# Kernel tuning notes

Hardware: AMD Instinct MI355X
Metric: run time of the kernel (lower is better)

The kernel has to match this reference:

```python
import math
import jax, jax.numpy as jnp
from jax import lax
import numpy as np

PATCHES = [(8, 8), (4, 4), (2, 2), (1, 1)]  # (width, height) per scale
BN_EPS = 1e-5


def setup_inputs() -> dict:
    key = jax.random.key(0)
    ks = jax.random.split(key, 9)
    b, d, h, w = 4, 256, 64, 64
    s = 1.0 / math.sqrt(d)
    return {
        "x": jax.random.normal(ks[0], (b, d, h, w), jnp.float32),
        "wq": jax.random.normal(ks[1], (d, d), jnp.float32) * s,
        "bq": jax.random.normal(ks[2], (d,), jnp.float32) * 0.02,
        "wk": jax.random.normal(ks[3], (d, d), jnp.float32) * s,
        "bk": jax.random.normal(ks[4], (d,), jnp.float32) * 0.02,
        "wv": jax.random.normal(ks[5], (d, d), jnp.float32) * s,
        "bv": jax.random.normal(ks[6], (d,), jnp.float32) * 0.02,
        "w_out": jax.random.normal(ks[7], (d, d, 3, 3), jnp.float32) * (s / 3.0),
        "b_out": jax.random.normal(ks[8], (d,), jnp.float32) * 0.02,
        "gamma": jnp.ones((d,), jnp.float32),
        "beta": jnp.zeros((d,), jnp.float32),
    }


def _to_tokens(t, b, dk, out_h, ph, out_w, pw):
    # [b, dk, h, w] -> [b, out_h*out_w, dk*ph*pw]
    t = t.reshape(b, dk, out_h, ph, out_w, pw)
    t = t.transpose(0, 2, 4, 1, 3, 5)
    return t.reshape(b, out_h * out_w, dk * ph * pw)


def reference(x, wq, bq, wk, bk, wv, bv, w_out, b_out, gamma, beta):
    b, c, h, w = x.shape
    # 1x1 conv projections == channel matmuls
    q = jnp.einsum('bchw,oc->bohw', x, wq) + bq[None, :, None, None]
    k = jnp.einsum('bchw,oc->bohw', x, wk) + bk[None, :, None, None]
    v = jnp.einsum('bchw,oc->bohw', x, wv) + bv[None, :, None, None]

    dk = c // len(PATCHES)
    outs = []
    for i, (pw, ph) in enumerate(PATCHES):
        sl = slice(i * dk, (i + 1) * dk)
        out_h, out_w = h // ph, w // pw
        Q = _to_tokens(q[:, sl], b, dk, out_h, ph, out_w, pw)
        K = _to_tokens(k[:, sl], b, dk, out_h, ph, out_w, pw)
        V = _to_tokens(v[:, sl], b, dk, out_h, ph, out_w, pw)
        scores = jnp.einsum('bnd,bmd->bnm', Q, K) / math.sqrt(Q.shape[-1])
        p = jax.nn.softmax(scores, axis=-1)
        y = jnp.einsum('bnm,bmd->bnd', p, V)
        # tokens -> [b, dk, h, w]
        y = y.reshape(b, out_h, out_w, dk, ph, pw)
        y = y.transpose(0, 3, 1, 4, 2, 5).reshape(b, dk, h, w)
        outs.append(y)
    out = jnp.concatenate(outs, axis=1)

    # 3x3 conv, padding=1
    z = lax.conv_general_dilated(out, w_out, (1, 1), 'SAME',
                                 dimension_numbers=('NCHW', 'OIHW', 'NCHW'))
    z = z + b_out[None, :, None, None]
    # BatchNorm2d (training-mode batch stats)
    mean = jnp.mean(z, axis=(0, 2, 3), keepdims=True)
    var = jnp.var(z, axis=(0, 2, 3), keepdims=True)
    zn = (z - mean) * lax.rsqrt(var + BN_EPS)
    zn = zn * gamma[None, :, None, None] + beta[None, :, None, None]
    # LeakyReLU(0.2)
    return jnp.where(zn > 0, zn, 0.2 * zn)
```

## Files before the change

kernel.cpp:

```cpp
#include <hip/hip_runtime.h>
#include <cmath>


#define OFF_XB  0LL
#define OFF_QB  2097152LL
#define OFF_SS  8388608LL
#define OFF_PP  12582912LL
#define OFF_YT  14680064LL
#define OFF_WQK 18874368LL
#define OFF_BIA 18972672LL
#define OFF_WCV 18973440LL
#define OFF_STT 19268352LL

#define FC 0.18033688f
#define CSHIFT 6.0f

typedef __attribute__((ext_vector_type(8))) short short8;
typedef __attribute__((ext_vector_type(4))) float f32x4;

__device__ inline unsigned short f2bf(float f) {
  unsigned u = __float_as_uint(f);
  u += 0x7fff + ((u >> 16) & 1);
  return (unsigned short)(u >> 16);
}

__device__ inline unsigned cvt_pk_bf16(float a, float b) {
  unsigned r;
  asm("v_cvt_pk_bf16_f32 %0, %1, %2" : "=v"(r) : "v"(a), "v"(b));
  return r;
}

__global__ __launch_bounds__(256) void xpose_k(
    const float* __restrict__ x, unsigned short* __restrict__ xb)
{
  __shared__ unsigned short rowb[256][66];
  const int b = blockIdx.x >> 6, y = blockIdx.x & 63;
  const int t = threadIdx.x;
  for (int i = t; i < 16384; i += 256) {
    int c = i >> 6, xx = i & 63;
    rowb[c][xx] = f2bf(x[((long long)(b*256 + c) << 12) + (y << 6) + xx]);
  }
  __syncthreads();
  unsigned int* outw = (unsigned int*)(xb + ((long long)blockIdx.x << 14));
  for (int i = t; i < 8192; i += 256) {
    int xx = i >> 7, c2 = (i & 127) * 2;
    outw[xx*128 + (c2 >> 1)] = (unsigned)rowb[c2][xx]
                             | ((unsigned)rowb[c2+1][xx] << 16);
  }
}

__global__ __launch_bounds__(256) void wcvt_k(
    const float* __restrict__ wq, const float* __restrict__ wk,
    const float* __restrict__ wv, const float* __restrict__ bq,
    const float* __restrict__ bk, const float* __restrict__ bv,
    unsigned short* __restrict__ Wqkv, float* __restrict__ biasQKV)
{
  const int row = blockIdx.x, t = threadIdx.x;
  const int which = row >> 8, oc = row & 255;
  const float* src = which == 0 ? wq : which == 1 ? wk : wv;
  Wqkv[row*256 + t] = f2bf(src[oc*256 + t]);
  if (row < 3) {
    const float* bs = row == 0 ? bq : row == 1 ? bk : bv;
    biasQKV[row*256 + t] = bs[t];
  }
}

template<int EPI, int ONEW>
__global__ __launch_bounds__(ONEW ? 64 : 256) void gemm_nt_k(
    const unsigned short* __restrict__ A, const unsigned short* __restrict__ B,
    void* __restrict__ Cv, const float* __restrict__ bias,
    int M, int N, int K, int lda, int ldb, int ldc,
    long long sA, long long sB, long long sC, float alpha)
{
  const int t = threadIdx.x, l = t & 63;
  const int lr = l & 15, lg = l >> 4;
  const int w = ONEW ? 0 : (t >> 6);
  const int wm = w >> 1, wn = w & 1;
  const int bz = blockIdx.z;
  const int m0 = blockIdx.y*(ONEW ? 64 : 128) + wm*64;
  const int n0 = blockIdx.x*(ONEW ? 64 : 128) + wn*64;
  if (m0 >= M || n0 >= N) return;
  const unsigned short* Ab = A + (long long)bz*sA + (long long)(m0 + lr)*lda + lg*8;
  const unsigned short* Bb = B + (long long)bz*sB + (long long)(n0 + lr)*ldb + lg*8;

  f32x4 acc[4][4] = {};
#pragma unroll 2
  for (int kk = 0; kk < K; kk += 32) {
    short8 af[4], bf[4];
#pragma unroll
    for (int i = 0; i < 4; i++)
      af[i] = *(const short8*)(Ab + (long long)i*16*lda + kk);
#pragma unroll
    for (int i = 0; i < 4; i++)
      bf[i] = *(const short8*)(Bb + (long long)i*16*ldb + kk);
#pragma unroll
    for (int mf = 0; mf < 4; mf++)
#pragma unroll
      for (int nf = 0; nf < 4; nf++)
        acc[mf][nf] = __builtin_amdgcn_mfma_f32_16x16x32_bf16(
            af[mf], bf[nf], acc[mf][nf], 0, 0, 0);
  }

  if (EPI == 0) {
    float* C = (float*)Cv + (long long)bz*sC;
#pragma unroll
    for (int mf = 0; mf < 4; mf++)
#pragma unroll
      for (int r = 0; r < 4; r++) {
        const int row = m0 + mf*16 + lg*4 + r;
#pragma unroll
        for (int nf = 0; nf < 4; nf++)
          C[(long long)row*ldc + n0 + nf*16 + lr] = acc[mf][nf][r] * alpha;
      }
  } else {
    unsigned short* Qbase = (unsigned short*)Cv;
#pragma unroll
    for (int mf = 0; mf < 4; mf++)
#pragma unroll
      for (int r = 0; r < 4; r++) {
        const int gi = m0 + mf*16 + lg*4 + r;
        const int which = gi >> 8, ch = gi & 255;
        const int scale = ch >> 6, c = ch & 63;
        const int sh = 3 - scale, msk = (1 << sh) - 1;
        const bool tr = (which == 2);
        const float bb = bias[gi];
        unsigned short* dst = Qbase + (long long)which*4194304
                            + (long long)scale*1048576 + (long long)bz*262144;
#pragma unroll
        for (int nf = 0; nf < 4; nf++) {
          const int gj = n0 + nf*16 + lr;
          const int y = gj >> 6, xx = gj & 63;
          const int n = (y >> sh)*(64 >> sh) + (xx >> sh);
          const int d = (c << (2*sh)) + ((y & msk) << sh) + (xx & msk);
          const long long idx = tr
              ? (long long)d*(4096 >> (2*sh)) + n
              : (long long)n*(64 << (2*sh)) + d;
          dst[idx] = f2bf(acc[mf][nf][r] + bb);
        }
      }
  }
}

__global__ __launch_bounds__(256) void s0_scores_k(
    const unsigned short* __restrict__ Q, const unsigned short* __restrict__ K,
    float* __restrict__ Sp)
{
  __shared__ float red[3][64][64];
  const int t = threadIdx.x, l = t & 63, w = t >> 6;
  const int lr = l & 15, lg = l >> 4;
  const int b = blockIdx.x >> 3, ks = blockIdx.x & 7;
  const unsigned short* Qb = Q + (long long)b*262144;
  const unsigned short* Kb = K + (long long)b*262144;
  f32x4 acc[4][4] = {};
  const int k0 = ks*512 + w*128;
#pragma unroll
  for (int kk = k0; kk < k0 + 128; kk += 32) {
    short8 af[4], bf[4];
#pragma unroll
    for (int i = 0; i < 4; i++)
      af[i] = *(const short8*)(Qb + (long long)(i*16 + lr)*4096 + kk + lg*8);
#pragma unroll
    for (int i = 0; i < 4; i++)
      bf[i] = *(const short8*)(Kb + (long long)(i*16 + lr)*4096 + kk + lg*8);
#pragma unroll
    for (int mf = 0; mf < 4; mf++)
#pragma unroll
      for (int nf = 0; nf < 4; nf++)
        acc[mf][nf] = __builtin_amdgcn_mfma_f32_16x16x32_bf16(
            af[mf], bf[nf], acc[mf][nf], 0, 0, 0);
  }
  if (w > 0) {
#pragma unroll
    for (int mf = 0; mf < 4; mf++)
#pragma unroll
      for (int r = 0; r < 4; r++)
#pragma unroll
        for (int nf = 0; nf < 4; nf++)
          red[w-1][mf*16 + lg*4 + r][nf*16 + lr] = acc[mf][nf][r];
  }
  __syncthreads();
  if (w == 0) {
#pragma unroll
    for (int mf = 0; mf < 4; mf++)
#pragma unroll
      for (int r = 0; r < 4; r++) {
        const int row = mf*16 + lg*4 + r;
#pragma unroll
        for (int nf = 0; nf < 4; nf++) {
          const int col = nf*16 + lr;
          Sp[(((long long)(ks*4 + b)*64 + row) << 6) + col]
              = acc[mf][nf][r] + red[0][row][col] + red[1][row][col]
              + red[2][row][col];
        }
      }
  }
}

__global__ __launch_bounds__(256) void s0_softmax_k(
    const float* __restrict__ Sp, unsigned short* __restrict__ P)
{
  const int t = threadIdx.x, l = t & 63, w = t >> 6;
  const int row = blockIdx.x*4 + w;
  const int b = row >> 6, r = row & 63;
  float v = 0.f;
#pragma unroll
  for (int ks = 0; ks < 8; ks++)
    v += Sp[(((long long)(ks*4 + b)*64 + r) << 6) + l];
  v *= 0.015625f;
  float mx = v;
#pragma unroll
  for (int off = 1; off < 64; off <<= 1) mx = fmaxf(mx, __shfl_xor(mx, off, 64));
  float e = __expf(v - mx), sum = e;
#pragma unroll
  for (int off = 1; off < 64; off <<= 1) sum += __shfl_xor(sum, off, 64);
  P[(row << 6) + l] = f2bf(e / sum);
}

template<int CNT>
__global__ __launch_bounds__(256) void softmax_bf_k(
    const float* __restrict__ S, unsigned short* __restrict__ P)
{
  const int t = threadIdx.x, l = t & 63, w = t >> 6;
  const long long row = (long long)blockIdx.x*4 + w;
  const float* p = S + row*(CNT*64);
  unsigned short* o = P + row*(CNT*64);
  float v[CNT];
  float mx = -1e30f;
#pragma unroll
  for (int i = 0; i < CNT; i++) { v[i] = p[i*64 + l]; mx = fmaxf(mx, v[i]); }
#pragma unroll
  for (int off = 1; off < 64; off <<= 1) mx = fmaxf(mx, __shfl_xor(mx, off, 64));
  float sum = 0.f;
#pragma unroll
  for (int i = 0; i < CNT; i++) { v[i] = __expf(v[i] - mx); sum += v[i]; }
#pragma unroll
  for (int off = 1; off < 64; off <<= 1) sum += __shfl_xor(sum, off, 64);
  const float inv = 1.f / sum;
#pragma unroll
  for (int i = 0; i < CNT; i++) o[i*64 + l] = f2bf(v[i] * inv);
}

__global__ __launch_bounds__(256) void flash3_mfma_k(
    const unsigned short* __restrict__ Q3, const unsigned short* __restrict__ K3,
    const unsigned short* __restrict__ Vt3, float* __restrict__ part,
    float* __restrict__ ml)
{
  constexpr int LD = 72;
  __shared__ unsigned short Ks[64*LD];
  __shared__ unsigned short Vs[64*LD];
  __shared__ unsigned short Ps[64*LD];
  const int t = threadIdx.x, l = t & 63, w = t >> 6;
  const int lr = l & 15, lg = l >> 4;
  const int b = blockIdx.y, q0 = blockIdx.x * 64, sp = blockIdx.z;
  const long long base = (long long)b * 262144;
  const unsigned short* Qg = Q3 + base;
  const unsigned short* Kg = K3 + base;
  const unsigned short* Vg = Vt3 + base;

  short8 bq[2];
  bq[0] = *(const short8*)(Qg + (long long)(q0 + w*16 + lr)*64 + lg*8);
  bq[1] = *(const short8*)(Qg + (long long)(q0 + w*16 + lr)*64 + 32 + lg*8);

  f32x4 acc[4] = {};
  float li = 0.f;

  const int r_ = t >> 3, c8_ = (t & 7) * 8;
  for (int kt = sp*16; kt < sp*16 + 16; kt++) {
    const int k0 = kt * 64;
    __syncthreads();
#pragma unroll
    for (int it = 0; it < 2; it++) {
      const int rr = r_ + it*32;
      *(uint4*)(Ks + rr*LD + c8_) =
          *(const uint4*)(Kg + (long long)(k0 + rr)*64 + c8_);
      *(uint4*)(Vs + rr*LD + c8_) =
          *(const uint4*)(Vg + (long long)rr*4096 + k0 + c8_);
    }
    __syncthreads();
    f32x4 s[4];
#pragma unroll
    for (int cf = 0; cf < 4; cf++) {
      short8 ak0 = *(const short8*)(Ks + (cf*16 + lr)*LD + lg*8);
      short8 ak1 = *(const short8*)(Ks + (cf*16 + lr)*LD + 32 + lg*8);
      f32x4 zz = {};
      zz = __builtin_amdgcn_mfma_f32_16x16x32_bf16(ak0, bq[0], zz, 0,0,0);
      s[cf] = __builtin_amdgcn_mfma_f32_16x16x32_bf16(ak1, bq[1], zz, 0,0,0);
    }
    float p[16];
    float psum = 0.f;
#pragma unroll
    for (int cf = 0; cf < 4; cf++)
#pragma unroll
      for (int r = 0; r < 4; r++) {
        float e = exp2f(fmaf(s[cf][r], FC, -CSHIFT));
        p[cf*4 + r] = e; psum += e;
      }
    li += psum;
    {
      unsigned short* pr = Ps + (w*16 + lr)*LD;
#pragma unroll
      for (int cf = 0; cf < 4; cf++) {
        *(unsigned*)(pr + cf*16 + lg*4)     = cvt_pk_bf16(p[cf*4+0], p[cf*4+1]);
        *(unsigned*)(pr + cf*16 + lg*4 + 2) = cvt_pk_bf16(p[cf*4+2], p[cf*4+3]);
      }
    }
    short8 bp0 = *(const short8*)(Ps + (w*16 + lr)*LD + lg*8);
    short8 bp1 = *(const short8*)(Ps + (w*16 + lr)*LD + 32 + lg*8);
#pragma unroll
    for (int df = 0; df < 4; df++) {
      short8 av0 = *(const short8*)(Vs + (df*16 + lr)*LD + lg*8);
      short8 av1 = *(const short8*)(Vs + (df*16 + lr)*LD + 32 + lg*8);
      acc[df] = __builtin_amdgcn_mfma_f32_16x16x32_bf16(av0, bp0, acc[df], 0,0,0);
      acc[df] = __builtin_amdgcn_mfma_f32_16x16x32_bf16(av1, bp1, acc[df], 0,0,0);
    }
  }
  li += __shfl_xor(li, 16);
  li += __shfl_xor(li, 32);
  const long long prow = (long long)(sp*4 + b)*4096 + q0 + w*16 + lr;
#pragma unroll
  for (int df = 0; df < 4; df++)
    *(float4*)(part + prow*64 + df*16 + lg*4) =
        make_float4(acc[df][0], acc[df][1], acc[df][2], acc[df][3]);
  if (lg == 0) ml[prow] = li;
}

__global__ __launch_bounds__(256) void fcomb_k(
    const float* __restrict__ part, const float* __restrict__ ml,
    unsigned short* __restrict__ inb)
{
  const int t = threadIdx.x;
  const long long row = (long long)blockIdx.x*64 + (t >> 2);
  const int dd = (t & 3) * 16;
  float L = 0.f;
#pragma unroll
  for (int s = 0; s < 4; s++) L += ml[(long long)s*16384 + row];
  const float inv = 1.f / L;
#pragma unroll
  for (int j = 0; j < 4; j++) {
    float ax = 0.f, ay = 0.f, az = 0.f, aw = 0.f;
#pragma unroll
    for (int s = 0; s < 4; s++) {
      float4 v = *(const float4*)(part + ((long long)s*16384 + row)*64 + dd + j*4);
      ax += v.x; ay += v.y; az += v.z; aw += v.w;
    }
    ushort4 ov;
    ov.x = f2bf(ax*inv); ov.y = f2bf(ay*inv);
    ov.z = f2bf(az*inv); ov.w = f2bf(aw*inv);
    *(ushort4*)(inb + row*256 + 192 + dd + j*4) = ov;
  }
}

__global__ __launch_bounds__(256) void unpack_nhwc_k(
    const float* __restrict__ Yt, unsigned short* __restrict__ inb)
{
  __shared__ unsigned short rowb[192][66];
  const int b = blockIdx.x >> 6, y = blockIdx.x & 63;
  const int t = threadIdx.x;
  for (int i = t; i < 12288; i += 256) {
    int ch = i >> 6, x = i & 63;
    int scale = ch >> 6, c = ch & 63;
    int sh = 3 - scale, msk = (1 << sh) - 1;
    int n = (y >> sh) * (64 >> sh) + (x >> sh);
    int d = (c << (2*sh)) + ((y & msk) << sh) + (x & msk);
    rowb[ch][x] = f2bf(Yt[(long long)scale*1048576 + ((long long)b << 18)
                          + (long long)n * (64 << (2*sh)) + d]);
  }
  __syncthreads();
  unsigned int* outw = (unsigned int*)(inb + ((long long)blockIdx.x << 14));
  for (int i = t; i < 6144; i += 256) {
    int xx = i / 96, cw = i % 96;
    outw[xx*128 + cw] = (unsigned)rowb[cw*2][xx]
                      | ((unsigned)rowb[cw*2+1][xx] << 16);
  }
}

__global__ __launch_bounds__(256) void wconv_k(
    const float* __restrict__ w, unsigned short* __restrict__ Wb)
{
  int i = blockIdx.x*256 + threadIdx.x;
  int tap = i >> 16, oc = (i >> 8) & 255, ic = i & 255;
  Wb[i] = f2bf(w[((long long)(oc*256 + ic))*9 + tap]);
}

__global__ __launch_bounds__(512) void conv_mfma_k(
    const unsigned short* __restrict__ inb, const unsigned short* __restrict__ Wb,
    const float* __restrict__ bias, float* __restrict__ z)
{
  __shared__ unsigned short lds[6*66*40];
  const int t = threadIdx.x;
  const int l = t & 63, wid = t >> 6;
  const int waveM = wid >> 2, waveN = wid & 3;
  const int tile = blockIdx.x;
  const int b = tile >> 4, y0 = (tile & 15) * 4;
  const int oc0 = blockIdx.y * 64 + waveM * 32;
  const long long inbase = (long long)b * 1048576;

  f32x4 acc[2][4] = {};

  const int kgrp = (l >> 4) * 8;
  for (int ic0 = 0; ic0 < 256; ic0 += 32) {
    __syncthreads();
    for (int q = t; q < 1584; q += 512) {
      int ic8 = q & 3, c = (q >> 2) % 66, r = q / 264;
      int gy = y0 - 1 + r, gx = c - 1;
      uint4 v = make_uint4(0u, 0u, 0u, 0u);
      if ((unsigned)gy < 64u && (unsigned)gx < 64u)
        v = *(const uint4*)(inb + inbase + ((long long)(gy*64 + gx))*256
                            + ic0 + ic8*8);
      *(uint4*)(lds + (q >> 2)*40 + ic8*8) = v;
    }
    __syncthreads();
    const unsigned short* wbase =
        Wb + (long long)(oc0 + (l & 15)) * 256 + ic0 + kgrp;
#pragma unroll
    for (int ky = 0; ky < 3; ky++) {
#pragma unroll
      for (int kx = 0; kx < 3; kx++) {
        const int tap = ky*3 + kx;
        short8 a0 = *(const short8*)(wbase + (long long)tap*65536);
        short8 a1 = *(const short8*)(wbase + (long long)tap*65536 + 16*256);
#pragma unroll
        for (int nf = 0; nf < 4; nf++) {
          int pix = waveN*64 + nf*16 + (l & 15);
          int rp = pix >> 6, x = pix & 63;
          short8 bf = *(const short8*)(lds + ((rp + ky)*66 + x + kx)*40 + kgrp);
          acc[0][nf] = __builtin_amdgcn_mfma_f32_16x16x32_bf16(a0, bf, acc[0][nf], 0, 0, 0);
          acc[1][nf] = __builtin_amdgcn_mfma_f32_16x16x32_bf16(a1, bf, acc[1][nf], 0, 0, 0);
        }
      }
    }
  }
  const long long zb = ((long long)b * 256) << 12;
#pragma unroll
  for (int mf = 0; mf < 2; mf++) {
#pragma unroll
    for (int r = 0; r < 4; r++) {
      const int oc = oc0 + mf*16 + (l >> 4)*4 + r;
      const float bb = bias[oc];
      const long long rowbase = zb + ((long long)oc << 12) + y0*64;
#pragma unroll
      for (int nf = 0; nf < 4; nf++) {
        int pix = waveN*64 + nf*16 + (l & 15);
        z[rowbase + pix] = acc[mf][nf][r] + bb;
      }
    }
  }
}

__global__ __launch_bounds__(256) void bn_stats_k(
    const float* __restrict__ z, float* __restrict__ stats)
{
  const int ch = blockIdx.x, t = threadIdx.x;
  float s = 0.f, q = 0.f;
  for (int b = 0; b < 4; b++) {
    const float* p = z + ((long long)(b*256 + ch) << 12);
    for (int i = t; i < 4096; i += 256) { float v = p[i]; s += v; q += v*v; }
  }
  __shared__ float rs[256], rq[256];
  rs[t] = s; rq[t] = q; __syncthreads();
  for (int st = 128; st > 0; st >>= 1) {
    if (t < st) { rs[t] += rs[t+st]; rq[t] += rq[t+st]; }
    __syncthreads();
  }
  if (t == 0) {
    float mean = rs[0] * (1.f/16384.f);
    float var  = rq[0] * (1.f/16384.f) - mean*mean;
    stats[ch]       = mean;
    stats[256 + ch] = rsqrtf(var + 1e-5f);
  }
}

__global__ __launch_bounds__(256) void bn_apply_k(
    const float* __restrict__ z, const float* __restrict__ stats,
    const float* __restrict__ gamma, const float* __restrict__ beta,
    float* __restrict__ out)
{
  long long i4 = ((long long)blockIdx.x*256 + threadIdx.x) * 4;
  int ch = (int)((i4 >> 12) & 255);
  float mean = stats[ch], rsg = stats[256 + ch];
  float g = gamma[ch], bt = beta[ch];
  float4 v = *(const float4*)(z + i4);
  float r[4] = {v.x, v.y, v.z, v.w};
#pragma unroll
  for (int j = 0; j < 4; j++) {
    float u = (r[j] - mean) * rsg * g + bt;
    r[j] = u > 0.f ? u : 0.2f * u;
  }
  *(float4*)(out + i4) = make_float4(r[0], r[1], r[2], r[3]);
}

extern "C" void kernel_launch(void* const* d_in, const int* in_sizes, int n_in,
                              void* d_out, int out_size, void* d_ws, size_t ws_size,
                              hipStream_t stream)
{
  const float* x     = (const float*)d_in[0];
  const float* wq    = (const float*)d_in[1];
  const float* bq    = (const float*)d_in[2];
  const float* wk    = (const float*)d_in[3];
  const float* bk    = (const float*)d_in[4];
  const float* wv    = (const float*)d_in[5];
  const float* bv    = (const float*)d_in[6];
  const float* w_out = (const float*)d_in[7];
  const float* b_out = (const float*)d_in[8];
  const float* gamma = (const float*)d_in[9];
  const float* beta  = (const float*)d_in[10];
  float* out = (float*)d_out;

  float* ws = (float*)d_ws;
  unsigned short* xb  = (unsigned short*)(ws + OFF_XB);
  unsigned short* Qu  = (unsigned short*)(ws + OFF_QB);
  unsigned short* Ku  = Qu + 4194304;
  unsigned short* Vu  = Qu + 8388608;
  float* SSf = ws + OFF_SS;
  unsigned short* PPu = (unsigned short*)(ws + OFF_PP);
  float* Yt  = ws + OFF_YT;
  unsigned short* Wqk = (unsigned short*)(ws + OFF_WQK);
  float* biasQ = ws + OFF_BIA;
  unsigned short* Wcv = (unsigned short*)(ws + OFF_WCV);
  float* St = ws + OFF_STT;
  unsigned short* inb = (unsigned short*)(ws + OFF_XB);
  float* z = Yt;

  dim3 blk(256);
  dim3 blk1(64);

  xpose_k<<<dim3(256), blk, 0, stream>>>(x, xb);
  wcvt_k<<<dim3(768), blk, 0, stream>>>(wq, wk, wv, bq, bk, bv, Wqk, biasQ);
  wconv_k<<<dim3(2304), blk, 0, stream>>>(w_out, Wcv);

  gemm_nt_k<1,0><<<dim3(32,6,4), blk, 0, stream>>>(
      Wqk, xb, (void*)Qu, biasQ, 768, 4096, 256, 256, 256, 0,
      0, 1048576, 0, 1.0f);

  s0_scores_k<<<dim3(32), blk, 0, stream>>>(Qu, Ku, SSf);
  s0_softmax_k<<<dim3(64), blk, 0, stream>>>(SSf, PPu);
  gemm_nt_k<0,1><<<dim3(64,1,4), blk1, 0, stream>>>(
      PPu, Vu, (void*)Yt, nullptr, 64, 4096, 64, 64, 64, 4096,
      4096, 262144, 262144, 1.0f);

  gemm_nt_k<0,1><<<dim3(4,4,4), blk1, 0, stream>>>(
      Qu+1048576, Ku+1048576, (void*)SSf, nullptr, 256, 256, 1024,
      1024, 1024, 256, 262144, 262144, 65536, 0.03125f);
  softmax_bf_k<4><<<dim3(256), blk, 0, stream>>>(SSf, PPu);
  gemm_nt_k<0,1><<<dim3(16,4,4), blk1, 0, stream>>>(
      PPu, Vu+1048576, (void*)(Yt+1048576), nullptr, 256, 1024, 256,
      256, 256, 1024, 65536, 262144, 262144, 1.0f);

  gemm_nt_k<0,0><<<dim3(8,8,4), blk, 0, stream>>>(
      Qu+2097152, Ku+2097152, (void*)SSf, nullptr, 1024, 1024, 256,
      256, 256, 1024, 262144, 262144, 1048576, 0.0625f);
  softmax_bf_k<16><<<dim3(1024), blk, 0, stream>>>(SSf, PPu);
  gemm_nt_k<0,1><<<dim3(4,16,4), blk1, 0, stream>>>(
      PPu, Vu+2097152, (void*)(Yt+2097152), nullptr, 1024, 256, 1024,
      1024, 1024, 256, 1048576, 262144, 262144, 1.0f);

  flash3_mfma_k<<<dim3(64,4,4), blk, 0, stream>>>(
      Qu+3145728, Ku+3145728, Vu+3145728, SSf, ws + OFF_PP);
  fcomb_k<<<dim3(256), blk, 0, stream>>>(SSf, ws + OFF_PP, inb);

  unpack_nhwc_k<<<dim3(256), blk, 0, stream>>>(Yt, inb);

  conv_mfma_k<<<dim3(64,4), dim3(512), 0, stream>>>(inb, Wcv, b_out, z);

  bn_stats_k<<<dim3(256), blk, 0, stream>>>(z, St);
  bn_apply_k<<<dim3(4096), blk, 0, stream>>>(z, St, gamma, beta, out);
}
```

Measured before the change: 266.7 us.

## Merge per-scale attention launches into staged multi-role kernels and double-buffer LDS loads

The separate prep kernels are merged into one launch. The per-scale score, softmax and PV kernels are grouped into three stage kernels that dispatch work by block index, so the scales run concurrently and launch count drops. The finest-scale flash attention now processes all keys in one block with register-staged double-buffered K/V, which removes the split-K partial buffers and the combine kernel. The 3x3 conv also gains double-buffered LDS and weights preloaded into registers. Risks include higher register pressure, lower parallelism for the flash blocks (256 blocks doing 64 iterations each), and load imbalance between the roles inside each stage kernel.

```diff
diff --git a/kernel.cpp b/kernel.cpp
--- a/kernel.cpp
+++ b/kernel.cpp
@@ -11,6 +11,10 @@
 #define OFF_BIA 18972672LL
 #define OFF_WCV 18973440LL
 #define OFF_STT 19268352LL
+#define OFF_SP0 19268864LL
+#define OFF_S1  19399936LL
+#define OFF_P0  19662080LL
+#define OFF_P1  19670272LL
 
 #define FC 0.18033688f
 #define CSHIFT 6.0f
@@ -30,55 +34,57 @@
   return r;
 }
 
-__global__ __launch_bounds__(256) void xpose_k(
-    const float* __restrict__ x, unsigned short* __restrict__ xb)
-{
-  __shared__ unsigned short rowb[256][66];
-  const int b = blockIdx.x >> 6, y = blockIdx.x & 63;
-  const int t = threadIdx.x;
-  for (int i = t; i < 16384; i += 256) {
-    int c = i >> 6, xx = i & 63;
-    rowb[c][xx] = f2bf(x[((long long)(b*256 + c) << 12) + (y << 6) + xx]);
-  }
-  __syncthreads();
-  unsigned int* outw = (unsigned int*)(xb + ((long long)blockIdx.x << 14));
-  for (int i = t; i < 8192; i += 256) {
-    int xx = i >> 7, c2 = (i & 127) * 2;
-    outw[xx*128 + (c2 >> 1)] = (unsigned)rowb[c2][xx]
-                             | ((unsigned)rowb[c2+1][xx] << 16);
-  }
-}
-
-__global__ __launch_bounds__(256) void wcvt_k(
+__global__ __launch_bounds__(256) void prep_k(
+    const float* __restrict__ x, unsigned short* __restrict__ xb,
     const float* __restrict__ wq, const float* __restrict__ wk,
     const float* __restrict__ wv, const float* __restrict__ bq,
     const float* __restrict__ bk, const float* __restrict__ bv,
-    unsigned short* __restrict__ Wqkv, float* __restrict__ biasQKV)
-{
-  const int row = blockIdx.x, t = threadIdx.x;
-  const int which = row >> 8, oc = row & 255;
-  const float* src = which == 0 ? wq : which == 1 ? wk : wv;
-  Wqkv[row*256 + t] = f2bf(src[oc*256 + t]);
-  if (row < 3) {
-    const float* bs = row == 0 ? bq : row == 1 ? bk : bv;
-    biasQKV[row*256 + t] = bs[t];
-  }
-}
-
-template<int EPI, int ONEW>
-__global__ __launch_bounds__(ONEW ? 64 : 256) void gemm_nt_k(
+    unsigned short* __restrict__ Wqkv, float* __restrict__ biasQKV,
+    const float* __restrict__ wcv, unsigned short* __restrict__ Wcb)
+{
+  const int bid = blockIdx.x, t = threadIdx.x;
+  if (bid < 256) {
+    __shared__ unsigned short rowb[256][66];
+    const int b = bid >> 6, y = bid & 63;
+    for (int i = t; i < 16384; i += 256) {
+      int c = i >> 6, xx = i & 63;
+      rowb[c][xx] = f2bf(x[((long long)(b*256 + c) << 12) + (y << 6) + xx]);
+    }
+    __syncthreads();
+    unsigned int* outw = (unsigned int*)(xb + ((long long)bid << 14));
+    for (int i = t; i < 8192; i += 256) {
+      int xx = i >> 7, c2 = (i & 127) * 2;
+      outw[xx*128 + (c2 >> 1)] = (unsigned)rowb[c2][xx]
+                               | ((unsigned)rowb[c2+1][xx] << 16);
+    }
+  } else if (bid < 1024) {
+    const int row = bid - 256;
+    const int which = row >> 8, oc = row & 255;
+    const float* src = which == 0 ? wq : which == 1 ? wk : wv;
+    Wqkv[row*256 + t] = f2bf(src[oc*256 + t]);
+    if (row < 3) {
+      const float* bs = row == 0 ? bq : row == 1 ? bk : bv;
+      biasQKV[row*256 + t] = bs[t];
+    }
+  } else {
+    int i = (bid - 1024)*256 + t;
+    int tap = i >> 16, oc = (i >> 8) & 255, ic = i & 255;
+    Wcb[i] = f2bf(wcv[((long long)(oc*256 + ic))*9 + tap]);
+  }
+}
+
+template<int EPI>
+__device__ void gemm_nt_body(
     const unsigned short* __restrict__ A, const unsigned short* __restrict__ B,
     void* __restrict__ Cv, const float* __restrict__ bias,
     int M, int N, int K, int lda, int ldb, int ldc,
-    long long sA, long long sB, long long sC, float alpha)
+    long long sA, long long sB, long long sC, float alpha,
+    int bx, int by, int bz)
 {
   const int t = threadIdx.x, l = t & 63;
   const int lr = l & 15, lg = l >> 4;
-  const int w = ONEW ? 0 : (t >> 6);
-  const int wm = w >> 1, wn = w & 1;
-  const int bz = blockIdx.z;
-  const int m0 = blockIdx.y*(ONEW ? 64 : 128) + wm*64;
-  const int n0 = blockIdx.x*(ONEW ? 64 : 128) + wn*64;
+  const int w = t >> 6, wm = w >> 1, wn = w & 1;
+  const int m0 = by*128 + wm*64, n0 = bx*128 + wn*64;
   if (m0 >= M || n0 >= N) return;
   const unsigned short* Ab = A + (long long)bz*sA + (long long)(m0 + lr)*lda + lg*8;
   const unsigned short* Bb = B + (long long)bz*sB + (long long)(n0 + lr)*ldb + lg*8;
@@ -141,20 +147,28 @@
   }
 }
 
-__global__ __launch_bounds__(256) void s0_scores_k(
+__global__ __launch_bounds__(256) void qkv_k(
+    const unsigned short* __restrict__ Wqkv, const unsigned short* __restrict__ xb,
+    unsigned short* __restrict__ Qu, const float* __restrict__ biasQKV)
+{
+  gemm_nt_body<1>(Wqkv, xb, (void*)Qu, biasQKV, 768, 4096, 256, 256, 256, 0,
+                  0, 1048576, 0, 1.0f, blockIdx.x, blockIdx.y, blockIdx.z);
+}
+
+__device__ void s0_scores_wave(
     const unsigned short* __restrict__ Q, const unsigned short* __restrict__ K,
-    float* __restrict__ Sp)
-{
-  __shared__ float red[3][64][64];
+    float* __restrict__ Sp, int bid)
+{
   const int t = threadIdx.x, l = t & 63, w = t >> 6;
   const int lr = l & 15, lg = l >> 4;
-  const int b = blockIdx.x >> 3, ks = blockIdx.x & 7;
+  const int task = bid*4 + w;
+  const int b = task >> 3, ks = task & 7;
   const unsigned short* Qb = Q + (long long)b*262144;
   const unsigned short* Kb = K + (long long)b*262144;
   f32x4 acc[4][4] = {};
-  const int k0 = ks*512 + w*128;
-#pragma unroll
-  for (int kk = k0; kk < k0 + 128; kk += 32) {
+  const int k0 = ks*512;
+#pragma unroll 2
+  for (int kk = k0; kk < k0 + 512; kk += 32) {
     short8 af[4], bf[4];
 #pragma unroll
     for (int i = 0; i < 4; i++)
@@ -169,89 +183,29 @@
         acc[mf][nf] = __builtin_amdgcn_mfma_f32_16x16x32_bf16(
             af[mf], bf[nf], acc[mf][nf], 0, 0, 0);
   }
-  if (w > 0) {
-#pragma unroll
-    for (int mf = 0; mf < 4; mf++)
-#pragma unroll
-      for (int r = 0; r < 4; r++)
-#pragma unroll
-        for (int nf = 0; nf < 4; nf++)
-          red[w-1][mf*16 + lg*4 + r][nf*16 + lr] = acc[mf][nf][r];
-  }
-  __syncthreads();
-  if (w == 0) {
-#pragma unroll
-    for (int mf = 0; mf < 4; mf++)
-#pragma unroll
-      for (int r = 0; r < 4; r++) {
-        const int row = mf*16 + lg*4 + r;
-#pragma unroll
-        for (int nf = 0; nf < 4; nf++) {
-          const int col = nf*16 + lr;
-          Sp[(((long long)(ks*4 + b)*64 + row) << 6) + col]
-              = acc[mf][nf][r] + red[0][row][col] + red[1][row][col]
-              + red[2][row][col];
-        }
-      }
-  }
-}
-
-__global__ __launch_bounds__(256) void s0_softmax_k(
-    const float* __restrict__ Sp, unsigned short* __restrict__ P)
-{
-  const int t = threadIdx.x, l = t & 63, w = t >> 6;
-  const int row = blockIdx.x*4 + w;
-  const int b = row >> 6, r = row & 63;
-  float v = 0.f;
-#pragma unroll
-  for (int ks = 0; ks < 8; ks++)
-    v += Sp[(((long long)(ks*4 + b)*64 + r) << 6) + l];
-  v *= 0.015625f;
-  float mx = v;
-#pragma unroll
-  for (int off = 1; off < 64; off <<= 1) mx = fmaxf(mx, __shfl_xor(mx, off, 64));
-  float e = __expf(v - mx), sum = e;
-#pragma unroll
-  for (int off = 1; off < 64; off <<= 1) sum += __shfl_xor(sum, off, 64);
-  P[(row << 6) + l] = f2bf(e / sum);
-}
-
-template<int CNT>
-__global__ __launch_bounds__(256) void softmax_bf_k(
-    const float* __restrict__ S, unsigned short* __restrict__ P)
-{
-  const int t = threadIdx.x, l = t & 63, w = t >> 6;
-  const long long row = (long long)blockIdx.x*4 + w;
-  const float* p = S + row*(CNT*64);
-  unsigned short* o = P + row*(CNT*64);
-  float v[CNT];
-  float mx = -1e30f;
-#pragma unroll
-  for (int i = 0; i < CNT; i++) { v[i] = p[i*64 + l]; mx = fmaxf(mx, v[i]); }
-#pragma unroll
-  for (int off = 1; off < 64; off <<= 1) mx = fmaxf(mx, __shfl_xor(mx, off, 64));
-  float sum = 0.f;
-#pragma unroll
-  for (int i = 0; i < CNT; i++) { v[i] = __expf(v[i] - mx); sum += v[i]; }
-#pragma unroll
-  for (int off = 1; off < 64; off <<= 1) sum += __shfl_xor(sum, off, 64);
-  const float inv = 1.f / sum;
-#pragma unroll
-  for (int i = 0; i < CNT; i++) o[i*64 + l] = f2bf(v[i] * inv);
-}
-
-__global__ __launch_bounds__(256) void flash3_mfma_k(
+#pragma unroll
+  for (int mf = 0; mf < 4; mf++)
+#pragma unroll
+    for (int r = 0; r < 4; r++) {
+      const int row = mf*16 + lg*4 + r;
+#pragma unroll
+      for (int nf = 0; nf < 4; nf++)
+        Sp[(((long long)(ks*4 + b)*64 + row) << 6) + nf*16 + lr]
+            = acc[mf][nf][r];
+    }
+}
+
+__device__ void flash3_body(
     const unsigned short* __restrict__ Q3, const unsigned short* __restrict__ K3,
-    const unsigned short* __restrict__ Vt3, float* __restrict__ part,
-    float* __restrict__ ml)
+    const unsigned short* __restrict__ Vt3, unsigned short* __restrict__ inb,
+    int bx, int b)
 {
   constexpr int LD = 72;
-  __shared__ unsigned short Ks[64*LD];
-  __shared__ unsigned short Vs[64*LD];
+  __shared__ unsigned short KVs[2][2][64*LD];
   __shared__ unsigned short Ps[64*LD];
   const int t = threadIdx.x, l = t & 63, w = t >> 6;
   const int lr = l & 15, lg = l >> 4;
-  const int b = blockIdx.y, q0 = blockIdx.x * 64, sp = blockIdx.z;
+  const int q0 = bx * 64;
   const long long base = (long long)b * 262144;
   const unsigned short* Qg = Q3 + base;
   const unsigned short* Kg = K3 + base;
@@ -265,29 +219,42 @@
   float li = 0.f;
 
   const int r_ = t >> 3, c8_ = (t & 7) * 8;
-  for (int kt = sp*16; kt < sp*16 + 16; kt++) {
-    const int k0 = kt * 64;
-    __syncthreads();
-#pragma unroll
-    for (int it = 0; it < 2; it++) {
-      const int rr = r_ + it*32;
-      *(uint4*)(Ks + rr*LD + c8_) =
-          *(const uint4*)(Kg + (long long)(k0 + rr)*64 + c8_);
-      *(uint4*)(Vs + rr*LD + c8_) =
-          *(const uint4*)(Vg + (long long)rr*4096 + k0 + c8_);
-    }
-    __syncthreads();
+  uint4 kreg[2], vreg[2];
+
+#define LOADKV(KT) do { \
+    const int k0_ = (KT) * 64; \
+    _Pragma("unroll") \
+    for (int it = 0; it < 2; it++) { \
+      const int rr = r_ + it*32; \
+      kreg[it] = *(const uint4*)(Kg + (long long)(k0_ + rr)*64 + c8_); \
+      vreg[it] = *(const uint4*)(Vg + (long long)rr*4096 + k0_ + c8_); \
+    } } while (0)
+#define STOREKV(BUF) do { \
+    _Pragma("unroll") \
+    for (int it = 0; it < 2; it++) { \
+      const int rr = r_ + it*32; \
+      *(uint4*)(KVs[BUF][0] + rr*LD + c8_) = kreg[it]; \
+      *(uint4*)(KVs[BUF][1] + rr*LD + c8_) = vreg[it]; \
+    } } while (0)
+
+  LOADKV(0);
+  STOREKV(0);
+  __syncthreads();
+
+  for (int kt = 0; kt < 64; ++kt) {
+    if (kt < 63) LOADKV(kt + 1);
+    const unsigned short* Ksb = KVs[kt & 1][0];
+    const unsigned short* Vsb = KVs[kt & 1][1];
     f32x4 s[4];
 #pragma unroll
     for (int cf = 0; cf < 4; cf++) {
-      short8 ak0 = *(const short8*)(Ks + (cf*16 + lr)*LD + lg*8);
-      short8 ak1 = *(const short8*)(Ks + (cf*16 + lr)*LD + 32 + lg*8);
+      short8 ak0 = *(const short8*)(Ksb + (cf*16 + lr)*LD + lg*8);
+      short8 ak1 = *(const short8*)(Ksb + (cf*16 + lr)*LD + 32 + lg*8);
       f32x4 zz = {};
       zz = __builtin_amdgcn_mfma_f32_16x16x32_bf16(ak0, bq[0], zz, 0,0,0);
       s[cf] = __builtin_amdgcn_mfma_f32_16x16x32_bf16(ak1, bq[1], zz, 0,0,0);
     }
-    float p[16];
-    float psum = 0.f;
+    float p[16], psum = 0.f;
 #pragma unroll
     for (int cf = 0; cf < 4; cf++)
 #pragma unroll
@@ -308,45 +275,128 @@
     short8 bp1 = *(const short8*)(Ps + (w*16 + lr)*LD + 32 + lg*8);
 #pragma unroll
     for (int df = 0; df < 4; df++) {
-      short8 av0 = *(const short8*)(Vs + (df*16 + lr)*LD + lg*8);
-      short8 av1 = *(const short8*)(Vs + (df*16 + lr)*LD + 32 + lg*8);
+      short8 av0 = *(const short8*)(Vsb + (df*16 + lr)*LD + lg*8);
+      short8 av1 = *(const short8*)(Vsb + (df*16 + lr)*LD + 32 + lg*8);
       acc[df] = __builtin_amdgcn_mfma_f32_16x16x32_bf16(av0, bp0, acc[df], 0,0,0);
       acc[df] = __builtin_amdgcn_mfma_f32_16x16x32_bf16(av1, bp1, acc[df], 0,0,0);
     }
-  }
+    if (kt < 63) {
+      STOREKV((kt + 1) & 1);
+      __syncthreads();
+    }
+  }
+#undef LOADKV
+#undef STOREKV
   li += __shfl_xor(li, 16);
   li += __shfl_xor(li, 32);
-  const long long prow = (long long)(sp*4 + b)*4096 + q0 + w*16 + lr;
-#pragma unroll
-  for (int df = 0; df < 4; df++)
-    *(float4*)(part + prow*64 + df*16 + lg*4) =
-        make_float4(acc[df][0], acc[df][1], acc[df][2], acc[df][3]);
-  if (lg == 0) ml[prow] = li;
-}
-
-__global__ __launch_bounds__(256) void fcomb_k(
-    const float* __restrict__ part, const float* __restrict__ ml,
+  const float inv = 1.f / li;
+  const long long row = (long long)b*4096 + q0 + w*16 + lr;
+  unsigned short* ob = inb + row*256 + 192 + lg*4;
+#pragma unroll
+  for (int df = 0; df < 4; df++) {
+    unsigned w0 = cvt_pk_bf16(acc[df][0]*inv, acc[df][1]*inv);
+    unsigned w1 = cvt_pk_bf16(acc[df][2]*inv, acc[df][3]*inv);
+    *(unsigned*)(ob + df*16)     = w0;
+    *(unsigned*)(ob + df*16 + 2) = w1;
+  }
+}
+
+__global__ __launch_bounds__(256) void stageA_k(
+    const unsigned short* __restrict__ Qu, const unsigned short* __restrict__ Ku,
+    const unsigned short* __restrict__ Vu,
+    float* __restrict__ Sp0, float* __restrict__ S1, float* __restrict__ S2,
     unsigned short* __restrict__ inb)
 {
-  const int t = threadIdx.x;
-  const long long row = (long long)blockIdx.x*64 + (t >> 2);
-  const int dd = (t & 3) * 16;
-  float L = 0.f;
-#pragma unroll
-  for (int s = 0; s < 4; s++) L += ml[(long long)s*16384 + row];
-  const float inv = 1.f / L;
-#pragma unroll
-  for (int j = 0; j < 4; j++) {
-    float ax = 0.f, ay = 0.f, az = 0.f, aw = 0.f;
-#pragma unroll
-    for (int s = 0; s < 4; s++) {
-      float4 v = *(const float4*)(part + ((long long)s*16384 + row)*64 + dd + j*4);
-      ax += v.x; ay += v.y; az += v.z; aw += v.w;
-    }
-    ushort4 ov;
-    ov.x = f2bf(ax*inv); ov.y = f2bf(ay*inv);
-    ov.z = f2bf(az*inv); ov.w = f2bf(aw*inv);
-    *(ushort4*)(inb + row*256 + 192 + dd + j*4) = ov;
+  const int bid = blockIdx.x;
+  if (bid < 256) {
+    flash3_body(Qu+3145728, Ku+3145728, Vu+3145728, inb, bid & 63, bid >> 6);
+  } else if (bid < 264) {
+    s0_scores_wave(Qu, Ku, Sp0, bid - 256);
+  } else if (bid < 280) {
+    int q = bid - 264;
+    gemm_nt_body<0>(Qu+1048576, Ku+1048576, (void*)S1, nullptr,
+        256, 256, 1024, 1024, 1024, 256, 262144, 262144, 65536, 0.03125f,
+        q & 1, (q >> 1) & 1, q >> 2);
+  } else {
+    int q = bid - 280;
+    gemm_nt_body<0>(Qu+2097152, Ku+2097152, (void*)S2, nullptr,
+        1024, 1024, 256, 256, 256, 1024, 262144, 262144, 1048576, 0.0625f,
+        q & 7, (q >> 3) & 7, q >> 6);
+  }
+}
+
+template<int CNT>
+__device__ void softmax_row(const float* __restrict__ S,
+                            unsigned short* __restrict__ P, long long row)
+{
+  const int l = threadIdx.x & 63;
+  const float* p = S + row*(CNT*64);
+  unsigned short* o = P + row*(CNT*64);
+  float v[CNT];
+  float mx = -1e30f;
+#pragma unroll
+  for (int i = 0; i < CNT; i++) { v[i] = p[i*64 + l]; mx = fmaxf(mx, v[i]); }
+#pragma unroll
+  for (int off = 1; off < 64; off <<= 1) mx = fmaxf(mx, __shfl_xor(mx, off, 64));
+  float sum = 0.f;
+#pragma unroll
+  for (int i = 0; i < CNT; i++) { v[i] = __expf(v[i] - mx); sum += v[i]; }
+#pragma unroll
+  for (int off = 1; off < 64; off <<= 1) sum += __shfl_xor(sum, off, 64);
+  const float inv = 1.f / sum;
+#pragma unroll
+  for (int i = 0; i < CNT; i++) o[i*64 + l] = f2bf(v[i] * inv);
+}
+
+__global__ __launch_bounds__(256) void stageB_k(
+    const float* __restrict__ Sp0, unsigned short* __restrict__ P0,
+    const float* __restrict__ S1, unsigned short* __restrict__ P1,
+    const float* __restrict__ S2, unsigned short* __restrict__ P2)
+{
+  const int bid = blockIdx.x, t = threadIdx.x, l = t & 63, w = t >> 6;
+  if (bid < 1024) {
+    softmax_row<16>(S2, P2, (long long)bid*4 + w);
+  } else if (bid < 1280) {
+    softmax_row<4>(S1, P1, (long long)(bid - 1024)*4 + w);
+  } else {
+    const int row = (bid - 1280)*4 + w;
+    const int b = row >> 6, r = row & 63;
+    float v = 0.f;
+#pragma unroll
+    for (int ks = 0; ks < 8; ks++)
+      v += Sp0[(((long long)(ks*4 + b)*64 + r) << 6) + l];
+    v *= 0.015625f;
+    float mx = v;
+#pragma unroll
+    for (int off = 1; off < 64; off <<= 1) mx = fmaxf(mx, __shfl_xor(mx, off, 64));
+    float e = __expf(v - mx), sum = e;
+#pragma unroll
+    for (int off = 1; off < 64; off <<= 1) sum += __shfl_xor(sum, off, 64);
+    P0[(row << 6) + l] = f2bf(e / sum);
+  }
+}
+
+__global__ __launch_bounds__(256) void stageC_k(
+    const unsigned short* __restrict__ P0, const unsigned short* __restrict__ P1,
+    const unsigned short* __restrict__ P2, const unsigned short* __restrict__ Vu,
+    float* __restrict__ Yt)
+{
+  const int bid = blockIdx.x;
+  if (bid < 128) {
+    int q = bid;
+    gemm_nt_body<0>(P0, Vu, (void*)Yt, nullptr,
+        64, 4096, 64, 64, 64, 4096, 4096, 262144, 262144, 1.0f,
+        q & 31, 0, q >> 5);
+  } else if (bid < 192) {
+    int q = bid - 128;
+    gemm_nt_body<0>(P1, Vu+1048576, (void*)(Yt+1048576), nullptr,
+        256, 1024, 256, 256, 256, 1024, 65536, 262144, 262144, 1.0f,
+        q & 7, (q >> 3) & 1, q >> 4);
+  } else {
+    int q = bid - 192;
+    gemm_nt_body<0>(P2, Vu+2097152, (void*)(Yt+2097152), nullptr,
+        1024, 256, 1024, 1024, 1024, 256, 1048576, 262144, 262144, 1.0f,
+        q & 1, (q >> 1) & 7, q >> 4);
   }
 }
 
@@ -374,73 +424,95 @@
   }
 }
 
-__global__ __launch_bounds__(256) void wconv_k(
-    const float* __restrict__ w, unsigned short* __restrict__ Wb)
-{
-  int i = blockIdx.x*256 + threadIdx.x;
-  int tap = i >> 16, oc = (i >> 8) & 255, ic = i & 255;
-  Wb[i] = f2bf(w[((long long)(oc*256 + ic))*9 + tap]);
-}
-
 __global__ __launch_bounds__(512) void conv_mfma_k(
     const unsigned short* __restrict__ inb, const unsigned short* __restrict__ Wb,
     const float* __restrict__ bias, float* __restrict__ z)
 {
-  __shared__ unsigned short lds[6*66*40];
+  __shared__ unsigned short lds[2][6*66*32];
   const int t = threadIdx.x;
   const int l = t & 63, wid = t >> 6;
+  const int lr = l & 15, lg = l >> 4;
   const int waveM = wid >> 2, waveN = wid & 3;
-  const int tile = blockIdx.x;
-  const int b = tile >> 4, y0 = (tile & 15) * 4;
+  const int b = blockIdx.x >> 4, y0 = (blockIdx.x & 15) * 4;
   const int oc0 = blockIdx.y * 64 + waveM * 32;
   const long long inbase = (long long)b * 1048576;
+  const int kgrp = lg * 8;
 
   f32x4 acc[2][4] = {};
-
-  const int kgrp = (l >> 4) * 8;
-  for (int ic0 = 0; ic0 < 256; ic0 += 32) {
-    __syncthreads();
-    for (int q = t; q < 1584; q += 512) {
-      int ic8 = q & 3, c = (q >> 2) % 66, r = q / 264;
-      int gy = y0 - 1 + r, gx = c - 1;
-      uint4 v = make_uint4(0u, 0u, 0u, 0u);
-      if ((unsigned)gy < 64u && (unsigned)gx < 64u)
-        v = *(const uint4*)(inb + inbase + ((long long)(gy*64 + gx))*256
-                            + ic0 + ic8*8);
-      *(uint4*)(lds + (q >> 2)*40 + ic8*8) = v;
-    }
-    __syncthreads();
-    const unsigned short* wbase =
-        Wb + (long long)(oc0 + (l & 15)) * 256 + ic0 + kgrp;
+  uint4 sreg[4];
+
+#define CLOAD(IC0) do { \
+    _Pragma("unroll") \
+    for (int i = 0; i < 4; i++) { \
+      int q = t + i*512; \
+      if (q < 1584) { \
+        int ic8 = q & 3, cc = (q >> 2) % 66, rr = q / 264; \
+        int gy = y0 - 1 + rr, gx = cc - 1; \
+        uint4 v = make_uint4(0u,0u,0u,0u); \
+        if ((unsigned)gy < 64u && (unsigned)gx < 64u) \
+          v = *(const uint4*)(inb + inbase + ((long long)(gy*64+gx))*256 \
+                              + (IC0) + ic8*8); \
+        sreg[i] = v; \
+      } \
+    } } while (0)
+#define CSTORE(BUF) do { \
+    _Pragma("unroll") \
+    for (int i = 0; i < 4; i++) { \
+      int q = t + i*512; \
+      if (q < 1584) *(uint4*)(&lds[BUF][q*8]) = sreg[i]; \
+    } } while (0)
+
+  CLOAD(0);
+  CSTORE(0);
+  __syncthreads();
+
+  for (int c = 0; c < 8; ++c) {
+    const int ic0 = c * 32;
+    if (c < 7) CLOAD(ic0 + 32);
+    const unsigned short* wbase = Wb + (long long)(oc0 + lr)*256 + ic0 + kgrp;
+    short8 afr[9][2];
+#pragma unroll
+    for (int tap = 0; tap < 9; tap++) {
+      afr[tap][0] = *(const short8*)(wbase + (long long)tap*65536);
+      afr[tap][1] = *(const short8*)(wbase + (long long)tap*65536 + 16*256);
+    }
+    const unsigned short* L = lds[c & 1];
 #pragma unroll
     for (int ky = 0; ky < 3; ky++) {
 #pragma unroll
       for (int kx = 0; kx < 3; kx++) {
         const int tap = ky*3 + kx;
-        short8 a0 = *(const short8*)(wbase + (long long)tap*65536);
-        short8 a1 = *(const short8*)(wbase + (long long)tap*65536 + 16*256);
 #pragma unroll
         for (int nf = 0; nf < 4; nf++) {
-          int pix = waveN*64 + nf*16 + (l & 15);
-          int rp = pix >> 6, x = pix & 63;
-          short8 bf = *(const short8*)(lds + ((rp + ky)*66 + x + kx)*40 + kgrp);
-          acc[0][nf] = __builtin_amdgcn_mfma_f32_16x16x32_bf16(a0, bf, acc[0][nf], 0, 0, 0);
-          acc[1][nf] = __builtin_amdgcn_mfma_f32_16x16x32_bf16(a1, bf, acc[1][nf], 0, 0, 0);
+          int pix = waveN*64 + nf*16 + lr;
+          int rp = pix >> 6, xx = pix & 63;
+          short8 bf = *(const short8*)(L + ((rp + ky)*66 + xx + kx)*32 + kgrp);
+          acc[0][nf] = __builtin_amdgcn_mfma_f32_16x16x32_bf16(
+              afr[tap][0], bf, acc[0][nf], 0, 0, 0);
+          acc[1][nf] = __builtin_amdgcn_mfma_f32_16x16x32_bf16(
+              afr[tap][1], bf, acc[1][nf], 0, 0, 0);
         }
       }
     }
-  }
+    if (c < 7) {
+      CSTORE((c + 1) & 1);
+      __syncthreads();
+    }
+  }
+#undef CLOAD
+#undef CSTORE
+
   const long long zb = ((long long)b * 256) << 12;
 #pragma unroll
   for (int mf = 0; mf < 2; mf++) {
 #pragma unroll
     for (int r = 0; r < 4; r++) {
-      const int oc = oc0 + mf*16 + (l >> 4)*4 + r;
+      const int oc = oc0 + mf*16 + lg*4 + r;
       const float bb = bias[oc];
       const long long rowbase = zb + ((long long)oc << 12) + y0*64;
 #pragma unroll
       for (int nf = 0; nf < 4; nf++) {
-        int pix = waveN*64 + nf*16 + (l & 15);
+        int pix = waveN*64 + nf*16 + lr;
         z[rowbase + pix] = acc[mf][nf][r] + bb;
       }
     }
@@ -511,52 +583,32 @@
   unsigned short* Qu  = (unsigned short*)(ws + OFF_QB);
   unsigned short* Ku  = Qu + 4194304;
   unsigned short* Vu  = Qu + 8388608;
-  float* SSf = ws + OFF_SS;
-  unsigned short* PPu = (unsigned short*)(ws + OFF_PP);
+  float* S2  = ws + OFF_SS;
+  unsigned short* P2 = (unsigned short*)(ws + OFF_PP);
   float* Yt  = ws + OFF_YT;
   unsigned short* Wqk = (unsigned short*)(ws + OFF_WQK);
   float* biasQ = ws + OFF_BIA;
   unsigned short* Wcv = (unsigned short*)(ws + OFF_WCV);
-  float* St = ws + OFF_STT;
+  float* St  = ws + OFF_STT;
+  float* Sp0 = ws + OFF_SP0;
+  float* S1  = ws + OFF_S1;
+  unsigned short* P0 = (unsigned short*)(ws + OFF_P0);
+  unsigned short* P1 = (unsigned short*)(ws + OFF_P1);
   unsigned short* inb = (unsigned short*)(ws + OFF_XB);
   float* z = Yt;
 
   dim3 blk(256);
-  dim3 blk1(64);
-
-  xpose_k<<<dim3(256), blk, 0, stream>>>(x, xb);
-  wcvt_k<<<dim3(768), blk, 0, stream>>>(wq, wk, wv, bq, bk, bv, Wqk, biasQ);
-  wconv_k<<<dim3(2304), blk, 0, stream>>>(w_out, Wcv);
-
-  gemm_nt_k<1,0><<<dim3(32,6,4), blk, 0, stream>>>(
-      Wqk, xb, (void*)Qu, biasQ, 768, 4096, 256, 256, 256, 0,
-      0, 1048576, 0, 1.0f);
-
-  s0_scores_k<<<dim3(32), blk, 0, stream>>>(Qu, Ku, SSf);
-  s0_softmax_k<<<dim3(64), blk, 0, stream>>>(SSf, PPu);
-  gemm_nt_k<0,1><<<dim3(64,1,4), blk1, 0, stream>>>(
-      PPu, Vu, (void*)Yt, nullptr, 64, 4096, 64, 64, 64, 4096,
-      4096, 262144, 262144, 1.0f);
-
-  gemm_nt_k<0,1><<<dim3(4,4,4), blk1, 0, stream>>>(
-      Qu+1048576, Ku+1048576, (void*)SSf, nullptr, 256, 256, 1024,
-      1024, 1024, 256, 262144, 262144, 65536, 0.03125f);
-  softmax_bf_k<4><<<dim3(256), blk, 0, stream>>>(SSf, PPu);
-  gemm_nt_k<0,1><<<dim3(16,4,4), blk1, 0, stream>>>(
-      PPu, Vu+1048576, (void*)(Yt+1048576), nullptr, 256, 1024, 256,
-      256, 256, 1024, 65536, 262144, 262144, 1.0f);
-
-  gemm_nt_k<0,0><<<dim3(8,8,4), blk, 0, stream>>>(
-      Qu+2097152, Ku+2097152, (void*)SSf, nullptr, 1024, 1024, 256,
-      256, 256, 1024, 262144, 262144, 1048576, 0.0625f);
-  softmax_bf_k<16><<<dim3(1024), blk, 0, stream>>>(SSf, PPu);
-  gemm_nt_k<0,1><<<dim3(4,16,4), blk1, 0, stream>>>(
-      PPu, Vu+2097152, (void*)(Yt+2097152), nullptr, 1024, 256, 1024,
-      1024, 1024, 256, 1048576, 262144, 262144, 1.0f);
-
-  flash3_mfma_k<<<dim3(64,4,4), blk, 0, stream>>>(
-      Qu+3145728, Ku+3145728, Vu+3145728, SSf, ws + OFF_PP);
-  fcomb_k<<<dim3(256), blk, 0, stream>>>(SSf, ws + OFF_PP, inb);
+
+  prep_k<<<dim3(3328), blk, 0, stream>>>(
+      x, xb, wq, wk, wv, bq, bk, bv, Wqk, biasQ, w_out, Wcv);
+
+  qkv_k<<<dim3(32,6,4), blk, 0, stream>>>(Wqk, xb, Qu, biasQ);
+
+  stageA_k<<<dim3(536), blk, 0, stream>>>(Qu, Ku, Vu, Sp0, S1, S2, inb);
+
+  stageB_k<<<dim3(1344), blk, 0, stream>>>(Sp0, P0, S1, P1, S2, P2);
+
+  stageC_k<<<dim3(256), blk, 0, stream>>>(P0, P1, P2, Vu, Yt);
 
   unpack_nhwc_k<<<dim3(256), blk, 0, stream>>>(Yt, inb);
 
```

After: 244.2 us. 8.4% less time.
